# Performance work log

Hardware: AMD Instinct MI355X
Metric: run time of the kernel (lower is better)

Reference implementation:

```python
import jax, jax.numpy as jnp
import numpy as np

# ---- config (matches init_kwargs) ----
C_IN, C_OUT = 128, 128
HYPER_OUT = 64            # hyper_out_size in DoubleConv
KB = C_IN // HYPER_OUT    # k = 2 blocks along input channels
HB = C_OUT // HYPER_OUT   # h = 2 blocks along output channels
Z_DIM, HID, SEIDEL_DIM = 128, 128, 48
R, F = 8, 3               # num_radii, filter size
BN_EPS = 1e-5


def _mlp_bank(z, W1, b1, W2, b2):
    # z: (S,); W1: (M,S,HID); returns (M, HID) embeddings from M distinct MLPs
    h = jax.nn.relu(jnp.einsum('s,msh->mh', z, W1) + b1)
    return jax.nn.relu(jnp.einsum('mh,mhg->mg', h, W2) + b2)


def _hyper(e, hw2, hb2, hw1, hb1):
    # Ha-style hypernetwork: e (Z_DIM,) -> kernel (64, 64, R, F, F)
    h_in = (e @ hw2 + hb2).reshape(HYPER_OUT, Z_DIM)
    h_fin = h_in @ hw1 + hb1  # (64, 64*R*F*F)
    return h_fin.reshape(HYPER_OUT, HYPER_OUT, R, F, F)


def _assemble(kernels, rows, cols):
    # kernels: (rows*cols, 64, 64, R, F, F) -> (rows*64, cols*64, R, F, F)
    k = kernels.reshape(rows, cols, HYPER_OUT, HYPER_OUT, R, F, F)
    k = k.transpose(0, 2, 1, 3, 4, 5, 6)
    return k.reshape(rows * HYPER_OUT, cols * HYPER_OUT, R, F, F)


def _interp_radii(w, Wdim):
    # trilinear interpolate (R,F,F)->(Wdim,F,F); F->F is identity, so linear along R
    # align_corners=False (PyTorch default)
    src = (jnp.arange(Wdim, dtype=jnp.float32) + 0.5) * (R / Wdim) - 0.5
    src = jnp.clip(src, 0.0, R - 1.0)
    i0 = jnp.floor(src).astype(jnp.int32)
    i1 = jnp.minimum(i0 + 1, R - 1)
    t = (src - i0.astype(jnp.float32))[None, None, :, None, None]
    return w[:, :, i0] * (1.0 - t) + w[:, :, i1] * t  # (co, ci, Wdim, F, F)


def _lri_conv(x, w):
    # x: (c_in, H, W); w: (c_out, c_in, R, F, F); padding=1, k=3
    c_in, H, W = x.shape
    xp = jnp.concatenate([x[:, -1:, :], x, x[:, :1, :]], axis=1)  # circular pad H
    xp = jnp.pad(xp, ((0, 0), (0, 0), (1, 1)))                    # zero pad W
    # patches laid out (c, di, dj) to match F.unfold
    pat = jnp.stack([xp[:, di:di + H, dj:dj + W]
                     for di in range(3) for dj in range(3)], axis=1)  # (c_in, 9, H, W)
    pat = pat.reshape(c_in * 9, H, W).transpose(1, 2, 0)              # (H, W, c_in*9)
    wi = _interp_radii(w, W)                                          # (co, ci, W, F, F)
    wu = wi.transpose(0, 2, 1, 3, 4).reshape(w.shape[0], W, c_in * 9) # (co, W, ci*9)
    return jnp.einsum('hwj,cwj->chw', pat, wu)                        # (co, H, W)


def _bn_eval(x, gamma, beta):
    # eval-mode BatchNorm2d with running_mean=0, running_var=1
    scale = gamma / jnp.sqrt(1.0 + BN_EPS)
    return x * scale[:, None, None] + beta[:, None, None]


def setup_inputs() -> dict:
    key = jax.random.key(0)
    ks = jax.random.split(key, 20)
    B, H, W = 2, 256, 128
    n1 = HB * KB   # 4 MLPs for first conv
    n2 = HB * HB   # 4 MLPs for second conv
    inp = {
        'x': jax.random.normal(ks[0], (B, C_IN, H, W), jnp.float32),
        'seidel': jax.random.normal(ks[1], (B, SEIDEL_DIM), jnp.float32),
        'm1_W1': jax.random.normal(ks[2], (n1, SEIDEL_DIM, HID)) * 0.1,
        'm1_b1': jnp.zeros((n1, HID)),
        'm1_W2': jax.random.normal(ks[3], (n1, HID, HID)) * 0.08,
        'm1_b2': jnp.zeros((n1, HID)),
        'm2_W1': jax.random.normal(ks[4], (n2, SEIDEL_DIM, HID)) * 0.1,
        'm2_b1': jnp.zeros((n2, HID)),
        'm2_W2': jax.random.normal(ks[5], (n2, HID, HID)) * 0.08,
        'm2_b2': jnp.zeros((n2, HID)),
        'hyp_w2': jax.random.normal(ks[6], (Z_DIM, HYPER_OUT * Z_DIM)) * 0.02,
        'hyp_b2': jnp.zeros((HYPER_OUT * Z_DIM,)),
        'hyp_w1': jax.random.normal(ks[7], (Z_DIM, HYPER_OUT * R * F * F)) * 0.02,
        'hyp_b1': jnp.zeros((HYPER_OUT * R * F * F,)),
        'bn1_g': jnp.ones((C_OUT,)), 'bn1_b': jnp.zeros((C_OUT,)),
        'bn2_g': jnp.ones((C_OUT,)), 'bn2_b': jnp.zeros((C_OUT,)),
    }
    return inp


def reference(x, seidel, m1_W1, m1_b1, m1_W2, m1_b2, m2_W1, m2_b1, m2_W2, m2_b2,
              hyp_w2, hyp_b2, hyp_w1, hyp_b1, bn1_g, bn1_b, bn2_g, bn2_b):
    hyper = lambda e: _hyper(e, hyp_w2, hyp_b2, hyp_w1, hyp_b1)

    def one_sample(x_i, z_i):
        emb1 = _mlp_bank(z_i, m1_W1, m1_b1, m1_W2, m1_b2)   # (h*k, Z)
        w1 = _assemble(jax.vmap(hyper)(emb1), HB, KB)        # (c_out, c_in, R, F, F)
        emb2 = _mlp_bank(z_i, m2_W1, m2_b1, m2_W2, m2_b2)   # (h*h, Z)
        w2 = _assemble(jax.vmap(hyper)(emb2), HB, HB)        # (c_out, c_out, R, F, F)
        y = jax.nn.relu(_bn_eval(_lri_conv(x_i, w1), bn1_g, bn1_b))
        y = jax.nn.relu(_bn_eval(_lri_conv(y, w2), bn2_g, bn2_b))
        return y

    return jax.vmap(one_sample)(x, seidel)  # (B, c_out, H, W)
```

## Files before the change

### kernel.cpp

```cpp
#include <hip/hip_runtime.h>
#include <hip/hip_bf16.h>

typedef _Float16 f16;
typedef _Float16 half8 __attribute__((ext_vector_type(8)));
typedef _Float16 half4_t __attribute__((ext_vector_type(4)));
typedef float floatx16 __attribute__((ext_vector_type(16)));

__device__ __forceinline__ void gll16(const void* g, void* l) {
    __builtin_amdgcn_global_load_lds(
        (const __attribute__((address_space(1))) void*)g,
        (__attribute__((address_space(3))) void*)l, 16, 0, 0);
}

__global__ __launch_bounds__(256) void prep_kernel(
    const float* __restrict__ x, f16* __restrict__ xt, float4* __restrict__ zerop,
    const float* __restrict__ seidel,
    const float* __restrict__ m1W1, const float* __restrict__ m1b1,
    const float* __restrict__ m1W2, const float* __restrict__ m1b2,
    const float* __restrict__ m2W1, const float* __restrict__ m2b1,
    const float* __restrict__ m2W2, const float* __restrict__ m2b2,
    float* __restrict__ eout,
    const float* __restrict__ hw1, float* __restrict__ hw1t)
{
    int b = blockIdx.x;
    int tid = threadIdx.x;
    if (b < 512) {
        __shared__ f16 tileT[128*136];
        int h = b & 255, s = b >> 8;
        if (b == 0 && tid < 4) zerop[tid] = make_float4(0.f, 0.f, 0.f, 0.f);
        int cg = tid >> 5, q2 = tid & 31;
        const float* src = x + (size_t)s*4194304 + (size_t)h*128;
        for (int pass = 0; pass < 16; ++pass) {
            int c = pass*8 + cg;
            float4 v = *(const float4*)(src + (size_t)c*32768 + q2*4);
            tileT[(q2*4 + 0)*136 + c] = (f16)v.x;
            tileT[(q2*4 + 1)*136 + c] = (f16)v.y;
            tileT[(q2*4 + 2)*136 + c] = (f16)v.z;
            tileT[(q2*4 + 3)*136 + c] = (f16)v.w;
        }
        __syncthreads();
        int ww = tid >> 1, hf = tid & 1;
        const f16* srcT = &tileT[ww*136 + hf*64];
        f16* dst = xt + (((size_t)(s*128 + ww)*256 + h)*128) + hf*64;
        #pragma unroll
        for (int i = 0; i < 8; ++i)
            *(float4*)(dst + i*8) = *(const float4*)(srcT + i*8);
    } else if (b < 528) {
        int combo = b - 512;
        int s = combo >> 3, conv = (combo >> 2) & 1, m = combo & 3;
        const float* W1 = conv ? m2W1 : m1W1;
        const float* b1 = conv ? m2b1 : m1b1;
        const float* W2 = conv ? m2W2 : m1W2;
        const float* b2 = conv ? m2b2 : m1b2;
        __shared__ float zs[48], hbuf[128];
        if (tid < 48) zs[tid] = seidel[s*48 + tid];
        __syncthreads();
        if (tid < 128) {
            float a = b1[m*128 + tid];
            for (int i = 0; i < 48; ++i) a += zs[i] * W1[(m*48 + i)*128 + tid];
            hbuf[tid] = fmaxf(a, 0.f);
        }
        __syncthreads();
        if (tid < 128) {
            float a = b2[m*128 + tid];
            for (int i = 0; i < 128; ++i) a += hbuf[i] * W2[(m*128 + i)*128 + tid];
            eout[combo*128 + tid] = fmaxf(a, 0.f);
        }
    } else {
        __shared__ float tile[32][33];
        int idx = b - 528;
        int j0 = (idx % 144)*32, k0 = (idx / 144)*32;
        int tx = tid & 31, ty = tid >> 5;
        #pragma unroll
        for (int i = 0; i < 4; ++i)
            tile[ty + i*8][tx] = hw1[(size_t)(k0 + ty + i*8)*4608 + j0 + tx];
        __syncthreads();
        #pragma unroll
        for (int i = 0; i < 4; ++i)
            hw1t[(size_t)(j0 + ty + i*8)*128 + k0 + tx] = tile[tx][ty + i*8];
    }
}

__global__ __launch_bounds__(128) void embed_b3(
    const float* __restrict__ eout, const float* __restrict__ hw2,
    const float* __restrict__ hb2, float* __restrict__ hin)
{
    __shared__ float es[16][128];
    int tid = threadIdx.x;
    int j = blockIdx.x*128 + tid;
    for (int i = tid; i < 2048; i += 128) es[i >> 7][i & 127] = eout[i];
    __syncthreads();
    float acc[16];
    float b = hb2[j];
    #pragma unroll
    for (int c = 0; c < 16; ++c) acc[c] = b;
    for (int i = 0; i < 128; ++i) {
        float wv = hw2[(size_t)i*8192 + j];
        #pragma unroll
        for (int c = 0; c < 16; ++c) acc[c] += es[c][i]*wv;
    }
    #pragma unroll
    for (int c = 0; c < 16; ++c) hin[(size_t)c*8192 + j] = acc[c];
}

__global__ __launch_bounds__(256) void hfin3_kernel(
    const float* __restrict__ hin, const float* __restrict__ hw1t,
    const float* __restrict__ hb1, f16* __restrict__ wtab)
{
    int c72 = blockIdx.x;
    int combo = blockIdx.y;
    int r = c72 / 9, tap = c72 - r*9;
    int s = combo >> 3, conv = (combo >> 2) & 1, m = combo & 3;
    __shared__ f16 A[64][136];
    __shared__ f16 B[64][136];
    __shared__ f16 ct[64][72];
    int tid = threadIdx.x;
    const float4* hsrc = (const float4*)(hin + (size_t)combo*8192);
    for (int i = tid; i < 2048; i += 256) {
        int a = i >> 5, k4 = (i & 31)*4;
        float4 v = hsrc[i];
        half4_t h; h[0]=(f16)v.x; h[1]=(f16)v.y; h[2]=(f16)v.z; h[3]=(f16)v.w;
        *(half4_t*)&A[a][k4] = h;
    }
    for (int i = tid; i < 2048; i += 256) {
        int b = i >> 5, k4 = (i & 31)*4;
        float4 v = *(const float4*)(hw1t + (size_t)(b*72 + c72)*128 + k4);
        half4_t h; h[0]=(f16)v.x; h[1]=(f16)v.y; h[2]=(f16)v.z; h[3]=(f16)v.w;
        *(half4_t*)&B[b][k4] = h;
    }
    __syncthreads();
    int lane = tid & 63, wid = tid >> 6;
    int wa = wid & 1, wb = wid >> 1;
    int l31 = lane & 31, lq = lane >> 5;
    floatx16 c = (floatx16)0.f;
    #pragma unroll
    for (int k = 0; k < 8; ++k) {
        half8 af = *(const half8*)&A[wa*32 + l31][k*16 + lq*8];
        half8 bf = *(const half8*)&B[wb*32 + l31][k*16 + lq*8];
        c = __builtin_amdgcn_mfma_f32_32x32x16_f16(af, bf, c, 0, 0, 0);
    }
    int bcol = wb*32 + l31;
    float bias = hb1[bcol*72 + c72];
    #pragma unroll
    for (int rr = 0; rr < 16; ++rr) {
        int a = wa*32 + (rr & 3) + 8*(rr >> 2) + 4*lq;
        ct[a][bcol] = (f16)(c[rr] + bias);
    }
    __syncthreads();
    {
        int a = tid & 63, q = tid >> 6;
        int chunk = (m & 1)*2 + (q >> 1);
        int co = (m >> 1)*64 + a;
        f16* dst = wtab + (((((size_t)(s*2 + conv)*8 + r)*4 + chunk)*9 + tap)*128 + co)*32
                   + (q & 1)*16;
        *(half8*)(dst)     = *(const half8*)&ct[a][q*16];
        *(half8*)(dst + 8) = *(const half8*)&ct[a][q*16 + 8];
    }
}

__global__ void xpose_out(const float* __restrict__ in, float* __restrict__ out)
{
    __shared__ float tile[32][33];
    int sc = blockIdx.z;
    int w0 = blockIdx.x*32, h0 = blockIdx.y*32;
    int tx = threadIdx.x, ty = threadIdx.y;
    const float* src = in + ((size_t)sc*128 + w0)*256 + h0;
    #pragma unroll
    for (int i = 0; i < 4; ++i) tile[ty + i*8][tx] = src[(size_t)(ty + i*8)*256 + tx];
    __syncthreads();
    float* dst = out + ((size_t)sc*256 + h0)*128 + w0;
    #pragma unroll
    for (int i = 0; i < 4; ++i) dst[(size_t)(ty + i*8)*128 + tx] = tile[tx][ty + i*8];
}

template<int OUT_F16>
__global__ __launch_bounds__(512, 1) void conv_mfma14(
    const f16* __restrict__ xin,
    const f16* __restrict__ wtab,
    int conv,
    const float* __restrict__ bng, const float* __restrict__ bnb,
    void* __restrict__ outp,
    const float4* __restrict__ zerop)
{
    int b = blockIdx.x;
    int xcd = b & 7, i = b >> 3;
    int s = xcd >> 2;
    int w = (xcd & 3)*32 + i;
    const f16* xs  = xin  + (size_t)s*4194304;
    const f16* wts = wtab + (size_t)(s*2 + conv)*1179648;

    float fsrc = fminf(fmaxf((w + 0.5f)*0.0625f - 0.5f, 0.f), 7.f);
    int r0 = (int)fsrc, r1 = min(r0 + 1, 7);
    f16 th = (f16)(fsrc - (float)r0);

    __shared__ __align__(16) char sbuf[122880];

    int tid = threadIdx.x;
    int lane = tid & 63, wid = tid >> 6;
    int wc = wid & 1, wh = wid >> 1;
    int l31 = lane & 31, lq = lane >> 5;

    floatx16 acc[2][2];
    #pragma unroll
    for (int a = 0; a < 2; ++a)
        #pragma unroll
        for (int c = 0; c < 2; ++c) acc[a][c] = (floatx16)0.f;

    half8 wa[5], wb[5];

    auto loadw = [&](int hc) {
        int chunk = hc >> 1, half = hc & 1;
        #pragma unroll
        for (int p = 0; p < 5; ++p) {
            int sl = p*512 + tid;
            if (sl < 2304) {
                int tap = sl >> 8, rem = sl & 255;
                int part = rem >> 7, co = rem & 127;
                size_t off = (size_t)co*32 + half*16 + part*8;
                wa[p] = *(const half8*)(wts + (((size_t)(r0*4 + chunk)*9 + tap) << 12) + off);
                wb[p] = *(const half8*)(wts + (((size_t)(r1*4 + chunk)*9 + tap) << 12) + off);
            }
            asm volatile("" : "+v"(wa[p]), "+v"(wb[p]));
        }
    };
    auto stage_x = [&](int bsel, int hc) {
        char* xb = sbuf + 73728 + bsel*24576;
        #pragma unroll
        for (int it = 0; it < 3; ++it) {
            int id = it*512 + tid;
            int dj = id >> 9, part = (id >> 8) & 1, hp = id & 255;
            int wsg = w + dj - 1;
            const void* src = (wsg >= 0 && wsg < 128)
                ? (const void*)(xs + ((size_t)wsg*256 + hp)*128 + hc*16 + part*8)
                : (const void*)zerop;
            gll16(src, xb + (size_t)(it*512 + wid*64)*16);
        }
    };
    auto write_w = [&](int bsel) {
        char* wbase = sbuf + bsel*36864;
        #pragma unroll
        for (int p = 0; p < 5; ++p) {
            int sl = p*512 + tid;
            if (sl < 2304) {
                half8 o = wa[p] + (wb[p] - wa[p])*th;
                *(half8*)(wbase + (size_t)sl*16) = o;
            }
        }
    };

    loadw(0);
    stage_x(0, 0);
    write_w(0);
    __syncthreads();

    #pragma unroll 2
    for (int hc = 0; hc < 8; ++hc) {
        int cur = hc & 1;
        if (hc < 7) { loadw(hc + 1); stage_x(cur ^ 1, hc + 1); }
        const char* wbuf = sbuf + cur*36864;
        const f16* xb = (const f16*)(sbuf + 73728 + cur*24576);

        #pragma unroll
        for (int tap = 0; tap < 4; ++tap) {
            int di = tap/3, dj = tap - di*3;
            half8 af0 = *(const half8*)(wbuf + (size_t)(tap*256 + lq*128 + wc*64 + l31)*16);
            half8 af1 = *(const half8*)(wbuf + (size_t)(tap*256 + lq*128 + wc*64 + 32 + l31)*16);
            int h0 = wh*64 + l31 + di - 1;
            half8 bf0 = *(const half8*)(xb + (size_t)(dj*512 + lq*256 + (h0 & 255))*8);
            half8 bf1 = *(const half8*)(xb + (size_t)(dj*512 + lq*256 + ((h0 + 32) & 255))*8);
            acc[0][0] = __builtin_amdgcn_mfma_f32_32x32x16_f16(af0, bf0, acc[0][0], 0, 0, 0);
            acc[0][1] = __builtin_amdgcn_mfma_f32_32x32x16_f16(af0, bf1, acc[0][1], 0, 0, 0);
            acc[1][0] = __builtin_amdgcn_mfma_f32_32x32x16_f16(af1, bf0, acc[1][0], 0, 0, 0);
            acc[1][1] = __builtin_amdgcn_mfma_f32_32x32x16_f16(af1, bf1, acc[1][1], 0, 0, 0);
        }
        if (hc < 7) write_w(cur ^ 1);
        #pragma unroll
        for (int tap = 4; tap < 9; ++tap) {
            int di = tap/3, dj = tap - di*3;
            half8 af0 = *(const half8*)(wbuf + (size_t)(tap*256 + lq*128 + wc*64 + l31)*16);
            half8 af1 = *(const half8*)(wbuf + (size_t)(tap*256 + lq*128 + wc*64 + 32 + l31)*16);
            int h0 = wh*64 + l31 + di - 1;
            half8 bf0 = *(const half8*)(xb + (size_t)(dj*512 + lq*256 + (h0 & 255))*8);
            half8 bf1 = *(const half8*)(xb + (size_t)(dj*512 + lq*256 + ((h0 + 32) & 255))*8);
            acc[0][0] = __builtin_amdgcn_mfma_f32_32x32x16_f16(af0, bf0, acc[0][0], 0, 0, 0);
            acc[0][1] = __builtin_amdgcn_mfma_f32_32x32x16_f16(af0, bf1, acc[0][1], 0, 0, 0);
            acc[1][0] = __builtin_amdgcn_mfma_f32_32x32x16_f16(af1, bf0, acc[1][0], 0, 0, 0);
            acc[1][1] = __builtin_amdgcn_mfma_f32_32x32x16_f16(af1, bf1, acc[1][1], 0, 0, 0);
        }
        __syncthreads();
    }

    float rs = rsqrtf(1.f + 1e-5f);
    if (OUT_F16) {
        f16* otile = (f16*)sbuf;
        f16* yout = (f16*)outp + ((size_t)(s*128 + w)*256)*128;
        #pragma unroll
        for (int ph = 0; ph < 2; ++ph) {
            __syncthreads();
            if ((wh >> 1) == ph) {
                #pragma unroll
                for (int ct = 0; ct < 2; ++ct) {
                    #pragma unroll
                    for (int ht = 0; ht < 2; ++ht) {
                        int hrow = (wh & 1)*64 + ht*32 + l31;
                        #pragma unroll
                        for (int rq = 0; rq < 4; ++rq) {
                            int cb = wc*64 + ct*32 + rq*8 + lq*4;
                            float4 g4 = *(const float4*)&bng[cb];
                            float4 b4 = *(const float4*)&bnb[cb];
                            half4_t v;
                            #pragma unroll
                            for (int e = 0; e < 4; ++e) {
                                float g = (&g4.x)[e], bb = (&b4.x)[e];
                                v[e] = (f16)fmaxf(acc[ct][ht][rq*4 + e]*g*rs + bb, 0.f);
                            }
                            *(half4_t*)&otile[hrow*136 + cb] = v;
                        }
                    }
                }
            }
            __syncthreads();
            {
                int hrow = tid >> 2, qc = tid & 3;
                const f16* srcT = &otile[hrow*136 + qc*32];
                f16* d = yout + (size_t)(ph*128 + hrow)*128 + qc*32;
                #pragma unroll
                for (int k = 0; k < 4; ++k)
                    *(float4*)(d + k*8) = *(const float4*)(srcT + k*8);
            }
        }
    } else {
        #pragma unroll
        for (int ct = 0; ct < 2; ++ct) {
            #pragma unroll
            for (int ht = 0; ht < 2; ++ht) {
                int hrow = wh*64 + ht*32 + l31;
                #pragma unroll
                for (int r = 0; r < 16; ++r) {
                    int co = wc*64 + ct*32 + (r & 3) + 8*(r >> 2) + 4*lq;
                    float v = fmaxf(acc[ct][ht][r]*bng[co]*rs + bnb[co], 0.f);
                    ((float*)outp)[((size_t)(s*128 + co)*128 + w)*256 + hrow] = v;
                }
            }
        }
    }
}

extern "C" void kernel_launch(void* const* d_in, const int* in_sizes, int n_in,
                              void* d_out, int out_size, void* d_ws, size_t ws_size,
                              hipStream_t stream) {
    const float* x      = (const float*)d_in[0];
    const float* seidel = (const float*)d_in[1];
    const float* m1W1 = (const float*)d_in[2];
    const float* m1b1 = (const float*)d_in[3];
    const float* m1W2 = (const float*)d_in[4];
    const float* m1b2 = (const float*)d_in[5];
    const float* m2W1 = (const float*)d_in[6];
    const float* m2b1 = (const float*)d_in[7];
    const float* m2W2 = (const float*)d_in[8];
    const float* m2b2 = (const float*)d_in[9];
    const float* hw2  = (const float*)d_in[10];
    const float* hb2  = (const float*)d_in[11];
    const float* hw1  = (const float*)d_in[12];
    const float* hb1  = (const float*)d_in[13];
    const float* bn1g = (const float*)d_in[14];
    const float* bn1b = (const float*)d_in[15];
    const float* bn2g = (const float*)d_in[16];
    const float* bn2b = (const float*)d_in[17];
    float* outp = (float*)d_out;

    char* wsb = (char*)d_ws;
    f16*   wtab = (f16*)wsb;
    f16*   y1t  = (f16*)(wsb + 9437184);
    f16*   xt   = (f16*)(wsb + 26214400);
    float* y2t  = (float*)(wsb + 26214400);
    float4* zerop = (float4*)(wsb + 59768832);
    float* hin  = (float*)(wsb + 59769856);
    float* eout = (float*)(wsb + 60294144);
    float* hw1t = (float*)(wsb + 60302336);

    prep_kernel<<<1104, 256, 0, stream>>>(x, xt, zerop, seidel,
                                          m1W1, m1b1, m1W2, m1b2,
                                          m2W1, m2b1, m2W2, m2b2,
                                          eout, hw1, hw1t);
    embed_b3<<<64, 128, 0, stream>>>(eout, hw2, hb2, hin);
    hfin3_kernel<<<dim3(72, 16), 256, 0, stream>>>(hin, hw1t, hb1, wtab);
    conv_mfma14<1><<<256, 512, 0, stream>>>(xt, wtab, 0, bn1g, bn1b, (void*)y1t, zerop);
    conv_mfma14<0><<<256, 512, 0, stream>>>(y1t, wtab, 1, bn2g, bn2b, (void*)y2t, zerop);
    xpose_out<<<dim3(4, 8, 256), dim3(32, 8), 0, stream>>>(y2t, outp);
}
```

Baseline: 133.7 us.

## Deepen weight prefetch to two chunks and use manual waitcnt barriers in conv

The conv kernel now loads interpolation weights two channel-chunks ahead into registers and writes them to LDS at the start of each iteration, instead of mid-loop. The 9-tap MFMA loop is merged into one, and __syncthreads is replaced by explicit s_waitcnt vmcnt/lgkmcnt plus s_barrier, so outstanding global weight loads can stay in flight across the barrier. The goal is to hide global load latency behind MFMA work. This relies on hand-chosen vmcnt counts matching the issue order, which is fragile if the compiler reorders loads. Longer register lifetimes also raise register pressure.

Measured after the change: 138.0 us. 1.03x slower.

```diff
diff --git a/kernel.cpp b/kernel.cpp
--- a/kernel.cpp
+++ b/kernel.cpp
@@ -174,7 +174,7 @@
 }
 
 template<int OUT_F16>
-__global__ __launch_bounds__(512, 1) void conv_mfma14(
+__global__ __launch_bounds__(512, 1) void conv_mfma15(
     const f16* __restrict__ xin,
     const f16* __restrict__ wtab,
     int conv,
@@ -220,7 +220,6 @@
                 wa[p] = *(const half8*)(wts + (((size_t)(r0*4 + chunk)*9 + tap) << 12) + off);
                 wb[p] = *(const half8*)(wts + (((size_t)(r1*4 + chunk)*9 + tap) << 12) + off);
             }
-            asm volatile("" : "+v"(wa[p]), "+v"(wb[p]));
         }
     };
     auto stage_x = [&](int bsel, int hc) {
@@ -251,17 +250,23 @@
     loadw(0);
     stage_x(0, 0);
     write_w(0);
-    __syncthreads();
-
-    #pragma unroll 2
+    loadw(1);
+    asm volatile("s_waitcnt vmcnt(8)" ::: "memory");
+    asm volatile("s_waitcnt lgkmcnt(0)" ::: "memory");
+    __builtin_amdgcn_s_barrier();
+
     for (int hc = 0; hc < 8; ++hc) {
         int cur = hc & 1;
-        if (hc < 7) { loadw(hc + 1); stage_x(cur ^ 1, hc + 1); }
+        if (hc < 7) {
+            write_w(cur ^ 1);
+            stage_x(cur ^ 1, hc + 1);
+        }
+        if (hc < 6) loadw(hc + 2);
         const char* wbuf = sbuf + cur*36864;
         const f16* xb = (const f16*)(sbuf + 73728 + cur*24576);
 
         #pragma unroll
-        for (int tap = 0; tap < 4; ++tap) {
+        for (int tap = 0; tap < 9; ++tap) {
             int di = tap/3, dj = tap - di*3;
             half8 af0 = *(const half8*)(wbuf + (size_t)(tap*256 + lq*128 + wc*64 + l31)*16);
             half8 af1 = *(const half8*)(wbuf + (size_t)(tap*256 + lq*128 + wc*64 + 32 + l31)*16);
@@ -273,21 +278,13 @@
             acc[1][0] = __builtin_amdgcn_mfma_f32_32x32x16_f16(af1, bf0, acc[1][0], 0, 0, 0);
             acc[1][1] = __builtin_amdgcn_mfma_f32_32x32x16_f16(af1, bf1, acc[1][1], 0, 0, 0);
         }
-        if (hc < 7) write_w(cur ^ 1);
-        #pragma unroll
-        for (int tap = 4; tap < 9; ++tap) {
-            int di = tap/3, dj = tap - di*3;
-            half8 af0 = *(const half8*)(wbuf + (size_t)(tap*256 + lq*128 + wc*64 + l31)*16);
-            half8 af1 = *(const half8*)(wbuf + (size_t)(tap*256 + lq*128 + wc*64 + 32 + l31)*16);
-            int h0 = wh*64 + l31 + di - 1;
-            half8 bf0 = *(const half8*)(xb + (size_t)(dj*512 + lq*256 + (h0 & 255))*8);
-            half8 bf1 = *(const half8*)(xb + (size_t)(dj*512 + lq*256 + ((h0 + 32) & 255))*8);
-            acc[0][0] = __builtin_amdgcn_mfma_f32_32x32x16_f16(af0, bf0, acc[0][0], 0, 0, 0);
-            acc[0][1] = __builtin_amdgcn_mfma_f32_32x32x16_f16(af0, bf1, acc[0][1], 0, 0, 0);
-            acc[1][0] = __builtin_amdgcn_mfma_f32_32x32x16_f16(af1, bf0, acc[1][0], 0, 0, 0);
-            acc[1][1] = __builtin_amdgcn_mfma_f32_32x32x16_f16(af1, bf1, acc[1][1], 0, 0, 0);
-        }
-        __syncthreads();
+
+        if (hc < 7) {
+            if (hc < 6) asm volatile("s_waitcnt vmcnt(8)" ::: "memory");
+            else        asm volatile("s_waitcnt vmcnt(0)" ::: "memory");
+            asm volatile("s_waitcnt lgkmcnt(0)" ::: "memory");
+            __builtin_amdgcn_s_barrier();
+        }
     }
 
     float rs = rsqrtf(1.f + 1e-5f);
@@ -385,7 +382,7 @@
                                           eout, hw1, hw1t);
     embed_b3<<<64, 128, 0, stream>>>(eout, hw2, hb2, hin);
     hfin3_kernel<<<dim3(72, 16), 256, 0, stream>>>(hin, hw1t, hb1, wtab);
-    conv_mfma14<1><<<256, 512, 0, stream>>>(xt, wtab, 0, bn1g, bn1b, (void*)y1t, zerop);
-    conv_mfma14<0><<<256, 512, 0, stream>>>(y1t, wtab, 1, bn2g, bn2b, (void*)y2t, zerop);
+    conv_mfma15<1><<<256, 512, 0, stream>>>(xt, wtab, 0, bn1g, bn1b, (void*)y1t, zerop);
+    conv_mfma15<0><<<256, 512, 0, stream>>>(y1t, wtab, 1, bn2g, bn2b, (void*)y2t, zerop);
     xpose_out<<<dim3(4, 8, 256), dim3(32, 8), 0, stream>>>(y2t, outp);
 }
```
